# Kernel optimization log

Measured on AMD Instinct MI355X. Metric: run time of the kernel, lower is better.

## Reference

```python
import jax, jax.numpy as jnp
import numpy as np

D_MODEL = 1024
BATCH = 4
SEQ = 4096

def setup_inputs() -> dict:
    key = jax.random.key(0)
    k1, k2, k3, k4 = jax.random.split(key, 4)
    scale = 1.0 / np.sqrt(D_MODEL)
    return {
        "inp_emb": jax.random.normal(k1, (BATCH, SEQ, D_MODEL), dtype=jnp.float32),
        "Wq": jax.random.normal(k2, (D_MODEL, D_MODEL), dtype=jnp.float32) * scale,
        "Wk": jax.random.normal(k3, (D_MODEL, D_MODEL), dtype=jnp.float32) * scale,
        "Wv": jax.random.normal(k4, (D_MODEL, D_MODEL), dtype=jnp.float32) * scale,
    }

def reference(inp_emb, Wq, Wk, Wv):
    d_model = Wq.shape[0]
    # torch Linear (no bias): y = x @ W.T
    Q = jnp.einsum('bsd,ed->bse', inp_emb, Wq)
    K = jnp.einsum('bsd,ed->bse', inp_emb, Wk)
    V = jnp.einsum('bsd,ed->bse', inp_emb, Wv)
    scores = jnp.einsum('bqd,bkd->bqk', Q, K) / jnp.sqrt(jnp.float32(d_model))
    probs = jax.nn.softmax(scores, axis=2)
    return jnp.einsum('bqk,bkd->bqd', probs, V)
```

## Files before the change

### kernel.cpp

```cpp
#include <hip/hip_runtime.h>


typedef __bf16 bf16_t;
typedef __bf16 bf16x8 __attribute__((ext_vector_type(8)));
typedef float f32x4 __attribute__((ext_vector_type(4)));

typedef __attribute__((address_space(3))) void lds_void_t;
typedef __attribute__((address_space(1))) void gbl_void_t;

#define SEQ 4096
#define DM  1024

__global__ __launch_bounds__(256) void cast_f32_to_bf16(
    const float* __restrict__ in, bf16_t* __restrict__ out, int n8)
{
    int idx = blockIdx.x * 256 + threadIdx.x;
    if (idx >= n8) return;
    long i = (long)idx * 8;
    f32x4 a = *(const f32x4*)(in + i);
    f32x4 b = *(const f32x4*)(in + i + 4);
    bf16x8 o;
    o[0] = (bf16_t)a[0]; o[1] = (bf16_t)a[1]; o[2] = (bf16_t)a[2]; o[3] = (bf16_t)a[3];
    o[4] = (bf16_t)b[0]; o[5] = (bf16_t)b[1]; o[6] = (bf16_t)b[2]; o[7] = (bf16_t)b[3];
    *(bf16x8*)(out + i) = o;
}

__global__ __launch_bounds__(256) void cast3_w(
    const float* __restrict__ w0, const float* __restrict__ w1,
    const float* __restrict__ w2, bf16_t* __restrict__ out)
{
    const float* in = (blockIdx.z == 0) ? w0 : (blockIdx.z == 1) ? w1 : w2;
    long i = ((long)blockIdx.x * 256 + threadIdx.x) * 8;
    f32x4 a = *(const f32x4*)(in + i);
    f32x4 b = *(const f32x4*)(in + i + 4);
    bf16x8 o;
    o[0] = (bf16_t)a[0]; o[1] = (bf16_t)a[1]; o[2] = (bf16_t)a[2]; o[3] = (bf16_t)a[3];
    o[4] = (bf16_t)b[0]; o[5] = (bf16_t)b[1]; o[6] = (bf16_t)b[2]; o[7] = (bf16_t)b[3];
    *(bf16x8*)(out + (long)blockIdx.z * 1048576 + i) = o;
}

__global__ __launch_bounds__(256) void zero_f32(float* __restrict__ p, int n)
{
    int idx = blockIdx.x * 256 + threadIdx.x;
    if (idx < n) p[idx] = 0.f;
}

template <typename TOUT, int MODE>
__global__ __launch_bounds__(256, 4) void gemm_bt(
    const bf16_t* __restrict__ A, int lda, long sAz,
    const bf16_t* __restrict__ B, int ldb, long sBz,
    TOUT* __restrict__ C, int ldc, long sCz,
    int K, float scale, float* __restrict__ l, long sLz)
{
    __shared__ bf16_t As[128 * 32];
    __shared__ bf16_t Bs[128 * 32];

    A += (long)blockIdx.z * sAz;
    B += (long)blockIdx.z * sBz;
    C += (long)blockIdx.z * sCz;

    const int tid  = threadIdx.x;
    const int wave = tid >> 6;
    const int lane = tid & 63;
    const int m0 = blockIdx.x * 128;
    const int n0 = blockIdx.y * 128;
    const int wm = (wave >> 1) * 64;
    const int wn = (wave & 1) * 64;
    const int mrow = lane & 15;
    const int koff = (lane >> 4) * 8;

    f32x4 acc[4][4];
#pragma unroll
    for (int i = 0; i < 4; ++i)
#pragma unroll
        for (int j = 0; j < 4; ++j)
            acc[i][j] = (f32x4){0.f, 0.f, 0.f, 0.f};

    const int c0 = wave * 2;

    for (int k0 = 0; k0 < K; k0 += 32) {
#pragma unroll
        for (int t = 0; t < 2; ++t) {
            const int chunk = c0 + t;
            const int flat  = chunk * 64 + lane;
            const int row   = flat >> 2;
            const int kp    = (flat & 3) * 8;
            const bf16_t* ga = A + (long)(m0 + row) * lda + (k0 + kp);
            const bf16_t* gb = B + (long)(n0 + row) * ldb + (k0 + kp);
            __builtin_amdgcn_global_load_lds((const gbl_void_t*)ga,
                                             (lds_void_t*)(As + chunk * 512), 16, 0, 0);
            __builtin_amdgcn_global_load_lds((const gbl_void_t*)gb,
                                             (lds_void_t*)(Bs + chunk * 512), 16, 0, 0);
        }
        __syncthreads();

        bf16x8 af[4], bfr[4];
#pragma unroll
        for (int i = 0; i < 4; ++i)
            af[i] = *(const bf16x8*)(As + (wm + i * 16 + mrow) * 32 + koff);
#pragma unroll
        for (int j = 0; j < 4; ++j)
            bfr[j] = *(const bf16x8*)(Bs + (wn + j * 16 + mrow) * 32 + koff);
#pragma unroll
        for (int i = 0; i < 4; ++i)
#pragma unroll
            for (int j = 0; j < 4; ++j)
                acc[i][j] = __builtin_amdgcn_mfma_f32_16x16x32_bf16(af[i], bfr[j], acc[i][j], 0, 0, 0);
        __syncthreads();
    }

    const int col = lane & 15;
    const int r0  = (lane >> 4) * 4;

    if (MODE == 1) {
#pragma unroll
        for (int i = 0; i < 4; ++i)
#pragma unroll
            for (int r = 0; r < 4; ++r) {
                float s = 0.f;
#pragma unroll
                for (int j = 0; j < 4; ++j) {
                    float e = __expf(acc[i][j][r] * scale);
                    acc[i][j][r] = e;
                    s += e;
                }
                s += __shfl_xor(s, 1);
                s += __shfl_xor(s, 2);
                s += __shfl_xor(s, 4);
                s += __shfl_xor(s, 8);
                if (col == 0)
                    atomicAdd(&l[(long)blockIdx.z * sLz + m0 + wm + i * 16 + r0 + r], s);
            }
#pragma unroll
        for (int i = 0; i < 4; ++i)
#pragma unroll
            for (int j = 0; j < 4; ++j)
#pragma unroll
                for (int r = 0; r < 4; ++r)
                    C[(long)(m0 + wm + i * 16 + r0 + r) * ldc + (n0 + wn + j * 16 + col)] =
                        (TOUT)acc[i][j][r];
    } else if (MODE == 2) {
        float inv[4][4];
#pragma unroll
        for (int i = 0; i < 4; ++i)
#pragma unroll
            for (int r = 0; r < 4; ++r)
                inv[i][r] = scale / l[(long)blockIdx.z * sLz + m0 + wm + i * 16 + r0 + r];
#pragma unroll
        for (int i = 0; i < 4; ++i)
#pragma unroll
            for (int j = 0; j < 4; ++j)
#pragma unroll
                for (int r = 0; r < 4; ++r)
                    C[(long)(m0 + wm + i * 16 + r0 + r) * ldc + (n0 + wn + j * 16 + col)] =
                        (TOUT)(acc[i][j][r] * inv[i][r]);
    } else {
#pragma unroll
        for (int i = 0; i < 4; ++i)
#pragma unroll
            for (int j = 0; j < 4; ++j)
#pragma unroll
                for (int r = 0; r < 4; ++r)
                    C[(long)(m0 + wm + i * 16 + r0 + r) * ldc + (n0 + wn + j * 16 + col)] =
                        (TOUT)(acc[i][j][r] * scale);
    }
}

__device__ __forceinline__ float waveMax(float v)
{
#pragma unroll
    for (int o = 32; o > 0; o >>= 1) v = fmaxf(v, __shfl_xor(v, o));
    return v;
}
__device__ __forceinline__ float waveSum(float v)
{
#pragma unroll
    for (int o = 32; o > 0; o >>= 1) v += __shfl_xor(v, o);
    return v;
}

__global__ __launch_bounds__(256) void softmax_rows(bf16_t* __restrict__ S)
{
    const long row = blockIdx.x;
    bf16_t* p = S + row * SEQ;
    const int tid = threadIdx.x;

    float v[16];
    bf16x8 a0 = *(const bf16x8*)(p + tid * 16);
    bf16x8 a1 = *(const bf16x8*)(p + tid * 16 + 8);
#pragma unroll
    for (int i = 0; i < 8; ++i) { v[i] = (float)a0[i]; v[8 + i] = (float)a1[i]; }

    float m = -1e30f;
#pragma unroll
    for (int i = 0; i < 16; ++i) m = fmaxf(m, v[i]);

    __shared__ float redm[4];
    __shared__ float reds[4];
    m = waveMax(m);
    if ((tid & 63) == 0) redm[tid >> 6] = m;
    __syncthreads();
    m = fmaxf(fmaxf(redm[0], redm[1]), fmaxf(redm[2], redm[3]));

    float s = 0.f;
#pragma unroll
    for (int i = 0; i < 16; ++i) { v[i] = __expf(v[i] - m); s += v[i]; }
    s = waveSum(s);
    if ((tid & 63) == 0) reds[tid >> 6] = s;
    __syncthreads();
    s = reds[0] + reds[1] + reds[2] + reds[3];
    const float inv = 1.0f / s;

    bf16x8 o0, o1;
#pragma unroll
    for (int i = 0; i < 8; ++i) {
        o0[i] = (bf16_t)(v[i] * inv);
        o1[i] = (bf16_t)(v[8 + i] * inv);
    }
    *(bf16x8*)(p + tid * 16)     = o0;
    *(bf16x8*)(p + tid * 16 + 8) = o1;
}

__global__ __launch_bounds__(256) void transpose_bf16(
    const bf16_t* __restrict__ in, int ldin, long sInZ,
    bf16_t* __restrict__ out, int ldout, long sOutZ)
{
    in  += (long)blockIdx.z * sInZ;
    out += (long)blockIdx.z * sOutZ;
    __shared__ bf16_t t[32][33];
    const int tx = threadIdx.x;
    const int ty = threadIdx.y;
    const int x  = blockIdx.x * 32 + tx;
    const int y0 = blockIdx.y * 32;
#pragma unroll
    for (int i = 0; i < 4; ++i)
        t[ty + i * 8][tx] = in[(long)(y0 + ty + i * 8) * ldin + x];
    __syncthreads();
    const int xo = blockIdx.x * 32;
#pragma unroll
    for (int i = 0; i < 4; ++i)
        out[(long)(xo + ty + i * 8) * ldout + y0 + tx] = t[tx][ty + i * 8];
}

extern "C" void kernel_launch(void* const* d_in, const int* in_sizes, int n_in,
                              void* d_out, int out_size, void* d_ws, size_t ws_size,
                              hipStream_t stream)
{
    const float* X  = (const float*)d_in[0];
    const float* Wq = (const float*)d_in[1];
    const float* Wk = (const float*)d_in[2];
    const float* Wv = (const float*)d_in[3];
    float* out = (float*)d_out;
    char* ws = (char*)d_ws;

    if (ws_size >= (256ull << 20)) {
        bf16_t* Xbf  = (bf16_t*)ws;
        bf16_t* Vbf  = (bf16_t*)(ws + (32l << 20));
        bf16_t* Tbuf = (bf16_t*)(ws + (32l << 20));
        bf16_t* VT   = (bf16_t*)(ws + (64l << 20));
        bf16_t* Sbuf = (bf16_t*)(ws + (96l << 20));
        bf16_t* Wall = (bf16_t*)(ws + (224l << 20));
        bf16_t* WqT  = (bf16_t*)(ws + (230l << 20));
        bf16_t* WkT  = (bf16_t*)(ws + (232l << 20));
        bf16_t* Mt   = (bf16_t*)(ws + (234l << 20));
        float*  lbuf = (float*)(ws + (236l << 20));

        cast_f32_to_bf16<<<(16777216 / 8) / 256, 256, 0, stream>>>(X, Xbf, 16777216 / 8);
        cast3_w<<<dim3(512, 1, 3), 256, 0, stream>>>(Wq, Wk, Wv, Wall);

        transpose_bf16<<<dim3(32, 32, 2), dim3(32, 8), 0, stream>>>(
            Wall, DM, 1048576, WqT, DM, 1048576);

        gemm_bt<bf16_t, 0><<<dim3(8, 8, 1), 256, 0, stream>>>(
            WkT, DM, 0l, WqT, DM, 0l, Mt, DM, 0l, DM, 1.0f, nullptr, 0l);

        gemm_bt<bf16_t, 0><<<dim3(128, 8, 1), 256, 0, stream>>>(
            Xbf, DM, 0l, Wall + 2097152, DM, 0l, Vbf, DM, 0l, DM, 1.0f, nullptr, 0l);

        transpose_bf16<<<dim3(DM / 32, SEQ / 32, 4), dim3(32, 8), 0, stream>>>(
            Vbf, DM, (long)SEQ * DM, VT, SEQ, (long)DM * SEQ);

        gemm_bt<bf16_t, 0><<<dim3(128, 8, 1), 256, 0, stream>>>(
            Xbf, DM, 0l, Mt, DM, 0l, Tbuf, DM, 0l, DM, 1.0f, nullptr, 0l);

        zero_f32<<<64, 256, 0, stream>>>(lbuf, 4 * SEQ);

        gemm_bt<bf16_t, 1><<<dim3(32, 32, 4), 256, 0, stream>>>(
            Tbuf, DM, (long)SEQ * DM,
            Xbf, DM, (long)SEQ * DM,
            Sbuf, SEQ, (long)SEQ * SEQ, DM, 0.03125f, lbuf, SEQ);

        gemm_bt<float, 2><<<dim3(32, 8, 4), 256, 0, stream>>>(
            Sbuf, SEQ, (long)SEQ * SEQ,
            VT, SEQ, (long)DM * SEQ,
            out, DM, (long)SEQ * DM, SEQ, 1.0f, lbuf, SEQ);
    } else {
        bf16_t* Sbuf = (bf16_t*)ws;
        bf16_t* Xbf  = (bf16_t*)ws;
        bf16_t* Wall = (bf16_t*)(ws + (33l << 20));
        bf16_t* QKV  = (bf16_t*)(ws + (40l << 20));
        bf16_t* VT   = (bf16_t*)(ws + (137l << 20));

        cast_f32_to_bf16<<<(16777216 / 8) / 256, 256, 0, stream>>>(X, Xbf, 16777216 / 8);
        cast3_w<<<dim3(512, 1, 3), 256, 0, stream>>>(Wq, Wk, Wv, Wall);

        gemm_bt<bf16_t, 0><<<dim3(128, 24, 1), 256, 0, stream>>>(
            Xbf, DM, 0l, Wall, DM, 0l, QKV, 3072, 0l, DM, 1.0f, nullptr, 0l);

        for (int b = 0; b < 4; ++b) {
            const bf16_t* Qb = QKV + (long)b * SEQ * 3072;
            gemm_bt<bf16_t, 0><<<dim3(32, 32, 1), 256, 0, stream>>>(
                Qb, 3072, 0l, Qb + 1024, 3072, 0l, Sbuf, SEQ, 0l, DM, 0.03125f, nullptr, 0l);
            softmax_rows<<<SEQ, 256, 0, stream>>>(Sbuf);
            transpose_bf16<<<dim3(DM / 32, SEQ / 32, 1), dim3(32, 8), 0, stream>>>(
                Qb + 2048, 3072, 0l, VT, SEQ, 0l);
            gemm_bt<float, 0><<<dim3(32, 8, 1), 256, 0, stream>>>(
                Sbuf, SEQ, 0l, VT, SEQ, 0l, out + (long)b * SEQ * DM, DM, 0l, SEQ, 1.0f, nullptr, 0l);
        }
    }
}
```

Baseline: 561.9 us.

## Add 256x256-tile 8-wave GEMM with triple-buffered LDS and use it for big GEMMs

Introduces a new GEMM kernel with 256x256 output tiles, 512 threads (8 waves, each 128x64), and a three-stage LDS ring fed by direct global-to-LDS loads. Loads for the next stages are interleaved between two MFMA halves, and s_setprio is raised around the MFMA blocks. The four large GEMMs (V projection, X·M, the score GEMM with fused exp and row sums, and the PV GEMM) switch to it. The goal is higher arithmetic intensity and fewer global loads per FLOP. The cost is 96KB of LDS per block and 128 accumulator registers per thread, which may limit occupancy or cause spills. The 16x16x4 launch for the score GEMM also leaves fewer blocks per wave of scheduling.

```diff
diff --git a/kernel.cpp b/kernel.cpp
--- a/kernel.cpp
+++ b/kernel.cpp
@@ -166,6 +166,173 @@
     }
 }
 
+template <typename TOUT, int MODE>
+__global__ __launch_bounds__(512, 2) void gemm_bt256(
+    const bf16_t* __restrict__ A, int lda, long sAz,
+    const bf16_t* __restrict__ B, int ldb, long sBz,
+    TOUT* __restrict__ C, int ldc, long sCz,
+    int K, float scale, float* __restrict__ l, long sLz)
+{
+    __shared__ __align__(1024) char smem[98304];
+
+    A += (long)blockIdx.z * sAz;
+    B += (long)blockIdx.z * sBz;
+    C += (long)blockIdx.z * sCz;
+
+    const int tid  = threadIdx.x;
+    const int wave = tid >> 6;
+    const int lane = tid & 63;
+    const int m0 = blockIdx.x * 256;
+    const int n0 = blockIdx.y * 256;
+    const int wm = (wave >> 2) * 128;
+    const int wn = (wave & 3) * 64;
+
+    const int srow = wave * 16 + (lane >> 2);
+    const int skk  = ((lane & 3) * 8) ^ ((lane & 32) ? 16 : 0);
+    const bf16_t* gA0 = A + (long)(m0 + srow) * lda + skk;
+    const bf16_t* gA1 = A + (long)(m0 + srow + 128) * lda + skk;
+    const bf16_t* gB0 = B + (long)(n0 + srow) * ldb + skk;
+    const bf16_t* gB1 = B + (long)(n0 + srow + 128) * ldb + skk;
+    char* ldsA = smem + wave * 1024;
+    char* ldsB = smem + 49152 + wave * 1024;
+
+    auto stage_A = [&](int kt, int d) {
+        const int k0 = kt << 5;
+        __builtin_amdgcn_global_load_lds((const gbl_void_t*)(gA0 + k0),
+                                         (lds_void_t*)(ldsA + d * 16384), 16, 0, 0);
+        __builtin_amdgcn_global_load_lds((const gbl_void_t*)(gA1 + k0),
+                                         (lds_void_t*)(ldsA + d * 16384 + 8192), 16, 0, 0);
+    };
+    auto stage_B = [&](int kt, int d) {
+        const int k0 = kt << 5;
+        __builtin_amdgcn_global_load_lds((const gbl_void_t*)(gB0 + k0),
+                                         (lds_void_t*)(ldsB + d * 16384), 16, 0, 0);
+        __builtin_amdgcn_global_load_lds((const gbl_void_t*)(gB1 + k0),
+                                         (lds_void_t*)(ldsB + d * 16384 + 8192), 16, 0, 0);
+    };
+
+    const int kswz = ((lane >> 4) * 16) ^ ((lane & 8) ? 32 : 0);
+    const int aoff = (wm + (lane & 15)) * 64 + kswz;
+    const int boff = (wn + (lane & 15)) * 64 + kswz;
+
+    f32x4 acc[8][4];
+#pragma unroll
+    for (int i = 0; i < 8; ++i)
+#pragma unroll
+        for (int j = 0; j < 4; ++j)
+            acc[i][j] = (f32x4){0.f, 0.f, 0.f, 0.f};
+
+    const int NT = K >> 5;
+
+    stage_A(0, 0); stage_B(0, 0);
+    if (NT > 1) {
+        stage_A(1, 1); stage_B(1, 1);
+        asm volatile("s_waitcnt vmcnt(4)" ::: "memory");
+    } else {
+        asm volatile("s_waitcnt vmcnt(0)" ::: "memory");
+    }
+    __builtin_amdgcn_s_barrier();
+
+    int cur = 0, nxt = 2;
+    for (int t = 0; t < NT; ++t) {
+        const char* pa = smem + cur * 16384 + aoff;
+        const char* pb = smem + 49152 + cur * 16384 + boff;
+
+        bf16x8 bfr[4], af[4];
+#pragma unroll
+        for (int j = 0; j < 4; ++j) bfr[j] = *(const bf16x8*)(pb + j * 1024);
+#pragma unroll
+        for (int i = 0; i < 4; ++i) af[i] = *(const bf16x8*)(pa + i * 1024);
+        if (t + 2 < NT) stage_A(t + 2, nxt);
+        __builtin_amdgcn_s_setprio(1);
+#pragma unroll
+        for (int i = 0; i < 4; ++i)
+#pragma unroll
+            for (int j = 0; j < 4; ++j)
+                acc[i][j] = __builtin_amdgcn_mfma_f32_16x16x32_bf16(af[i], bfr[j], acc[i][j], 0, 0, 0);
+        __builtin_amdgcn_s_setprio(0);
+
+        bf16x8 af2[4];
+#pragma unroll
+        for (int i = 0; i < 4; ++i) af2[i] = *(const bf16x8*)(pa + 4096 + i * 1024);
+        if (t + 2 < NT) stage_B(t + 2, nxt);
+        __builtin_amdgcn_s_setprio(1);
+#pragma unroll
+        for (int i = 0; i < 4; ++i)
+#pragma unroll
+            for (int j = 0; j < 4; ++j)
+                acc[4 + i][j] = __builtin_amdgcn_mfma_f32_16x16x32_bf16(af2[i], bfr[j], acc[4 + i][j], 0, 0, 0);
+        __builtin_amdgcn_s_setprio(0);
+
+        __builtin_amdgcn_sched_barrier(0);
+        if (t + 2 < NT)
+            asm volatile("s_waitcnt vmcnt(4) lgkmcnt(0)" ::: "memory");
+        else if (t + 1 < NT)
+            asm volatile("s_waitcnt vmcnt(0) lgkmcnt(0)" ::: "memory");
+        else
+            asm volatile("s_waitcnt lgkmcnt(0)" ::: "memory");
+        __builtin_amdgcn_s_barrier();
+        cur = (cur == 2) ? 0 : cur + 1;
+        nxt = (nxt == 2) ? 0 : nxt + 1;
+    }
+
+    const int col = lane & 15;
+    const int r0  = (lane >> 4) * 4;
+
+    if (MODE == 1) {
+#pragma unroll
+        for (int i = 0; i < 8; ++i)
+#pragma unroll
+            for (int r = 0; r < 4; ++r) {
+                float s = 0.f;
+#pragma unroll
+                for (int j = 0; j < 4; ++j) {
+                    float e = __expf(acc[i][j][r] * scale);
+                    acc[i][j][r] = e;
+                    s += e;
+                }
+                s += __shfl_xor(s, 1);
+                s += __shfl_xor(s, 2);
+                s += __shfl_xor(s, 4);
+                s += __shfl_xor(s, 8);
+                if (col == 0)
+                    atomicAdd(&l[(long)blockIdx.z * sLz + m0 + wm + i * 16 + r0 + r], s);
+            }
+#pragma unroll
+        for (int i = 0; i < 8; ++i)
+#pragma unroll
+            for (int j = 0; j < 4; ++j)
+#pragma unroll
+                for (int r = 0; r < 4; ++r)
+                    C[(long)(m0 + wm + i * 16 + r0 + r) * ldc + (n0 + wn + j * 16 + col)] =
+                        (TOUT)acc[i][j][r];
+    } else if (MODE == 2) {
+        float inv[8][4];
+#pragma unroll
+        for (int i = 0; i < 8; ++i)
+#pragma unroll
+            for (int r = 0; r < 4; ++r)
+                inv[i][r] = scale / l[(long)blockIdx.z * sLz + m0 + wm + i * 16 + r0 + r];
+#pragma unroll
+        for (int i = 0; i < 8; ++i)
+#pragma unroll
+            for (int j = 0; j < 4; ++j)
+#pragma unroll
+                for (int r = 0; r < 4; ++r)
+                    C[(long)(m0 + wm + i * 16 + r0 + r) * ldc + (n0 + wn + j * 16 + col)] =
+                        (TOUT)(acc[i][j][r] * inv[i][r]);
+    } else {
+#pragma unroll
+        for (int i = 0; i < 8; ++i)
+#pragma unroll
+            for (int j = 0; j < 4; ++j)
+#pragma unroll
+                for (int r = 0; r < 4; ++r)
+                    C[(long)(m0 + wm + i * 16 + r0 + r) * ldc + (n0 + wn + j * 16 + col)] =
+                        (TOUT)(acc[i][j][r] * scale);
+    }
+}
+
 __device__ __forceinline__ float waveMax(float v)
 {
 #pragma unroll
@@ -274,23 +441,23 @@
         gemm_bt<bf16_t, 0><<<dim3(8, 8, 1), 256, 0, stream>>>(
             WkT, DM, 0l, WqT, DM, 0l, Mt, DM, 0l, DM, 1.0f, nullptr, 0l);
 
-        gemm_bt<bf16_t, 0><<<dim3(128, 8, 1), 256, 0, stream>>>(
+        gemm_bt256<bf16_t, 0><<<dim3(64, 4, 1), 512, 0, stream>>>(
             Xbf, DM, 0l, Wall + 2097152, DM, 0l, Vbf, DM, 0l, DM, 1.0f, nullptr, 0l);
 
         transpose_bf16<<<dim3(DM / 32, SEQ / 32, 4), dim3(32, 8), 0, stream>>>(
             Vbf, DM, (long)SEQ * DM, VT, SEQ, (long)DM * SEQ);
 
-        gemm_bt<bf16_t, 0><<<dim3(128, 8, 1), 256, 0, stream>>>(
+        gemm_bt256<bf16_t, 0><<<dim3(64, 4, 1), 512, 0, stream>>>(
             Xbf, DM, 0l, Mt, DM, 0l, Tbuf, DM, 0l, DM, 1.0f, nullptr, 0l);
 
         zero_f32<<<64, 256, 0, stream>>>(lbuf, 4 * SEQ);
 
-        gemm_bt<bf16_t, 1><<<dim3(32, 32, 4), 256, 0, stream>>>(
+        gemm_bt256<bf16_t, 1><<<dim3(16, 16, 4), 512, 0, stream>>>(
             Tbuf, DM, (long)SEQ * DM,
             Xbf, DM, (long)SEQ * DM,
             Sbuf, SEQ, (long)SEQ * SEQ, DM, 0.03125f, lbuf, SEQ);
 
-        gemm_bt<float, 2><<<dim3(32, 8, 4), 256, 0, stream>>>(
+        gemm_bt256<float, 2><<<dim3(16, 4, 4), 512, 0, stream>>>(
             Sbuf, SEQ, (long)SEQ * SEQ,
             VT, SEQ, (long)DM * SEQ,
             out, DM, (long)SEQ * DM, SEQ, 1.0f, lbuf, SEQ);
```

Result: faster. 519.0 us (-7.6%).
